# Kernel tuning notes

Hardware: AMD Instinct MI355X
Metric: run time of the kernel (lower is better)

## Reference

```python
import jax, jax.numpy as jnp
import numpy as np

NUM_SEGMENTS = 100000  # number of cycle slots (max cycle id + 1)


def setup_inputs() -> dict:
    key = jax.random.key(0)
    k1, k2, k3 = jax.random.split(key, 3)
    x = jax.random.randint(k1, (100000,), 0, 22, dtype=jnp.int64)
    atom_to_cycle = jax.random.randint(k2, (2, 600000), 0, NUM_SEGMENTS, dtype=jnp.int64)
    emb_weight = jax.random.normal(k3, (22, 128), dtype=jnp.float32)  # Embedding(22, hidden_dim)
    return {"x": x, "atom_to_cycle": atom_to_cycle, "emb_weight": emb_weight}


def reference(x, atom_to_cycle, emb_weight):
    # x: [N] int atom codes; atom_to_cycle: [2, E]; emb_weight: [22, D]
    h = emb_weight[x]                       # [N, D] embedding lookup
    gathered = h[atom_to_cycle[0]]          # [E, D] gather by atom index
    # scatter_sum over cycle ids -> [NUM_SEGMENTS, D]
    out = jax.ops.segment_sum(gathered, atom_to_cycle[1], num_segments=NUM_SEGMENTS)
    return out
```

## Files before the change

### kernel.cpp

```cpp
#include <hip/hip_runtime.h>
#include <stdint.h>

#define KCODES 22
#define KW     11

__global__ void zero_hist(uint32_t* __restrict__ cnt, int nwords4) {
    int i = blockIdx.x * blockDim.x + threadIdx.x;
    if (i < nwords4) {
        ((uint4*)cnt)[i] = make_uint4(0u, 0u, 0u, 0u);
    }
}

__global__ void count_edges(const int* __restrict__ a2c,
                            const int* __restrict__ x,
                            uint32_t* __restrict__ cnt, int E) {
    int e = blockIdx.x * blockDim.x + threadIdx.x;
    if (e < E) {
        int atom = a2c[e];
        int cyc  = a2c[E + e];
        int code = x[atom];
        atomicAdd(&cnt[cyc * KW + (code >> 1)], 1u << ((code & 1) * 16));
    }
}

__global__ __launch_bounds__(256) void expand_out(
        const uint32_t* __restrict__ cnt,
        const float* __restrict__ emb,
        float* __restrict__ out, int num_seg) {
    __shared__ float4 semb[KCODES][32];
    for (int i = threadIdx.x; i < KCODES * 32; i += blockDim.x) {
        semb[i >> 5][i & 31] = ((const float4*)emb)[i];
    }
    __syncthreads();

    const int d4  = threadIdx.x & 31;
    const int sub = threadIdx.x >> 5;

    int c = blockIdx.x * 8 + sub;
    if (c < num_seg) {
        const uint32_t* crow = cnt + (size_t)c * KW;
        float4 acc = make_float4(0.f, 0.f, 0.f, 0.f);
#pragma unroll
        for (int w = 0; w < KW; ++w) {
            uint32_t word = crow[w];
            float c0 = (float)(word & 0xFFFFu);
            float c1 = (float)(word >> 16);
            float4 e0 = semb[2 * w][d4];
            float4 e1 = semb[2 * w + 1][d4];
            acc.x += c0 * e0.x + c1 * e1.x;
            acc.y += c0 * e0.y + c1 * e1.y;
            acc.z += c0 * e0.z + c1 * e1.z;
            acc.w += c0 * e0.w + c1 * e1.w;
        }
        ((float4*)out)[(size_t)c * 32 + d4] = acc;
    }
}

__global__ void zero_out_f4(float4* __restrict__ out, int n4) {
    int i = blockIdx.x * blockDim.x + threadIdx.x;
    if (i < n4) out[i] = make_float4(0.f, 0.f, 0.f, 0.f);
}

__global__ void scatter_edges(const int* __restrict__ a2c,
                              const int* __restrict__ x,
                              const float* __restrict__ emb,
                              float* __restrict__ out, int E) {
    int t = blockIdx.x * blockDim.x + threadIdx.x;
    int e = t >> 5;
    int d = (t & 31) * 4;
    if (e < E) {
        int atom = a2c[e];
        int cyc  = a2c[E + e];
        int code = x[atom];
        const float4 ev = ((const float4*)emb)[code * 32 + (d >> 2)];
        float* o = out + (size_t)cyc * 128 + d;
        atomicAdd(o + 0, ev.x);
        atomicAdd(o + 1, ev.y);
        atomicAdd(o + 2, ev.z);
        atomicAdd(o + 3, ev.w);
    }
}

extern "C" void kernel_launch(void* const* d_in, const int* in_sizes, int n_in,
                              void* d_out, int out_size, void* d_ws, size_t ws_size,
                              hipStream_t stream) {
    const int*   x    = (const int*)d_in[0];
    const int*   a2c  = (const int*)d_in[1];
    const float* emb  = (const float*)d_in[2];
    float*       out  = (float*)d_out;

    const int E       = in_sizes[1] / 2;
    const int D       = in_sizes[2] / KCODES;
    const int num_seg = out_size / D;

    const size_t need = (size_t)num_seg * KW * sizeof(uint32_t);

    if (ws_size >= need) {
        uint32_t* cnt = (uint32_t*)d_ws;
        const int nwords  = num_seg * KW;
        const int nwords4 = (nwords + 3) / 4;

        zero_hist<<<(nwords4 + 255) / 256, 256, 0, stream>>>(cnt, nwords4);
        count_edges<<<(E + 255) / 256, 256, 0, stream>>>(a2c, x, cnt, E);
        expand_out<<<(num_seg + 7) / 8, 256, 0, stream>>>(cnt, emb, out, num_seg);
    } else {
        int n4 = out_size / 4;
        zero_out_f4<<<(n4 + 255) / 256, 256, 0, stream>>>((float4*)out, n4);
        long long threads = (long long)E * 32;
        int blocks = (int)((threads + 255) / 256);
        scatter_edges<<<blocks, 256, 0, stream>>>(a2c, x, emb, out, E);
    }
    (void)n_in; (void)D;
}
```

Before: 116.3 us.

## Pad histogram rows, vectorize edge counting, register-cache embeddings in expand

Pads each cycle's packed count row to 12 words so the expand kernel can read it with three 16-byte loads. The edge-counting kernel now handles four edges per thread using int4 loads, and the custom zero kernel is replaced by hipMemsetAsync. The expand kernel keeps all 22 embedding float4s in registers instead of shared memory, drops the barrier, and runs as a grid-stride loop capped at 2048 blocks. The extra padding word raises workspace traffic, and the 88 registers per thread used for the embedding table may lower occupancy.

```diff
diff --git a/kernel.cpp b/kernel.cpp
--- a/kernel.cpp
+++ b/kernel.cpp
@@ -2,24 +2,36 @@
 #include <stdint.h>
 
 #define KCODES 22
-#define KW     11
+#define KW     12
 
-__global__ void zero_hist(uint32_t* __restrict__ cnt, int nwords4) {
+__global__ void count_edges4(const int* __restrict__ a2c,
+                             const int* __restrict__ x,
+                             uint32_t* __restrict__ cnt, int E) {
     int i = blockIdx.x * blockDim.x + threadIdx.x;
-    if (i < nwords4) {
-        ((uint4*)cnt)[i] = make_uint4(0u, 0u, 0u, 0u);
+    int E4 = E >> 2;
+    if (i < E4) {
+        int4 a = ((const int4*)a2c)[i];
+        int4 c = ((const int4*)(a2c + E))[i];
+        uint32_t k0 = (uint32_t)x[a.x];
+        uint32_t k1 = (uint32_t)x[a.y];
+        uint32_t k2 = (uint32_t)x[a.z];
+        uint32_t k3 = (uint32_t)x[a.w];
+        atomicAdd(&cnt[(size_t)c.x * KW + (k0 >> 1)], 1u << ((k0 & 1) << 4));
+        atomicAdd(&cnt[(size_t)c.y * KW + (k1 >> 1)], 1u << ((k1 & 1) << 4));
+        atomicAdd(&cnt[(size_t)c.z * KW + (k2 >> 1)], 1u << ((k2 & 1) << 4));
+        atomicAdd(&cnt[(size_t)c.w * KW + (k3 >> 1)], 1u << ((k3 & 1) << 4));
     }
 }
 
-__global__ void count_edges(const int* __restrict__ a2c,
-                            const int* __restrict__ x,
-                            uint32_t* __restrict__ cnt, int E) {
+__global__ void count_edges1(const int* __restrict__ a2c,
+                             const int* __restrict__ x,
+                             uint32_t* __restrict__ cnt, int E) {
     int e = blockIdx.x * blockDim.x + threadIdx.x;
     if (e < E) {
         int atom = a2c[e];
         int cyc  = a2c[E + e];
-        int code = x[atom];
-        atomicAdd(&cnt[cyc * KW + (code >> 1)], 1u << ((code & 1) * 16));
+        uint32_t code = (uint32_t)x[atom];
+        atomicAdd(&cnt[(size_t)cyc * KW + (code >> 1)], 1u << ((code & 1) << 4));
     }
 }
 
@@ -27,30 +39,30 @@
         const uint32_t* __restrict__ cnt,
         const float* __restrict__ emb,
         float* __restrict__ out, int num_seg) {
-    __shared__ float4 semb[KCODES][32];
-    for (int i = threadIdx.x; i < KCODES * 32; i += blockDim.x) {
-        semb[i >> 5][i & 31] = ((const float4*)emb)[i];
-    }
-    __syncthreads();
-
     const int d4  = threadIdx.x & 31;
     const int sub = threadIdx.x >> 5;
 
-    int c = blockIdx.x * 8 + sub;
-    if (c < num_seg) {
-        const uint32_t* crow = cnt + (size_t)c * KW;
+    float4 e[KCODES];
+#pragma unroll
+    for (int k = 0; k < KCODES; ++k)
+        e[k] = ((const float4*)emb)[k * 32 + d4];
+
+    for (int c = blockIdx.x * 8 + sub; c < num_seg; c += gridDim.x * 8) {
+        const uint4* crow = (const uint4*)(cnt + (size_t)c * KW);
+        uint4 w0 = crow[0], w1 = crow[1], w2 = crow[2];
+        uint32_t wv[12] = {w0.x, w0.y, w0.z, w0.w,
+                           w1.x, w1.y, w1.z, w1.w,
+                           w2.x, w2.y, w2.z, w2.w};
         float4 acc = make_float4(0.f, 0.f, 0.f, 0.f);
 #pragma unroll
-        for (int w = 0; w < KW; ++w) {
-            uint32_t word = crow[w];
-            float c0 = (float)(word & 0xFFFFu);
-            float c1 = (float)(word >> 16);
-            float4 e0 = semb[2 * w][d4];
-            float4 e1 = semb[2 * w + 1][d4];
-            acc.x += c0 * e0.x + c1 * e1.x;
-            acc.y += c0 * e0.y + c1 * e1.y;
-            acc.z += c0 * e0.z + c1 * e1.z;
-            acc.w += c0 * e0.w + c1 * e1.w;
+        for (int w = 0; w < 11; ++w) {
+            float c0 = (float)(wv[w] & 0xFFFFu);
+            float c1 = (float)(wv[w] >> 16);
+            float4 e0 = e[2 * w], e1 = e[2 * w + 1];
+            acc.x = fmaf(c1, e1.x, fmaf(c0, e0.x, acc.x));
+            acc.y = fmaf(c1, e1.y, fmaf(c0, e0.y, acc.y));
+            acc.z = fmaf(c1, e1.z, fmaf(c0, e0.z, acc.z));
+            acc.w = fmaf(c1, e1.w, fmaf(c0, e0.w, acc.w));
         }
         ((float4*)out)[(size_t)c * 32 + d4] = acc;
     }
@@ -97,12 +109,19 @@
 
     if (ws_size >= need) {
         uint32_t* cnt = (uint32_t*)d_ws;
-        const int nwords  = num_seg * KW;
-        const int nwords4 = (nwords + 3) / 4;
 
-        zero_hist<<<(nwords4 + 255) / 256, 256, 0, stream>>>(cnt, nwords4);
-        count_edges<<<(E + 255) / 256, 256, 0, stream>>>(a2c, x, cnt, E);
-        expand_out<<<(num_seg + 7) / 8, 256, 0, stream>>>(cnt, emb, out, num_seg);
+        hipMemsetAsync(cnt, 0, need, stream);
+
+        if ((E & 3) == 0) {
+            int E4 = E >> 2;
+            count_edges4<<<(E4 + 255) / 256, 256, 0, stream>>>(a2c, x, cnt, E);
+        } else {
+            count_edges1<<<(E + 255) / 256, 256, 0, stream>>>(a2c, x, cnt, E);
+        }
+
+        int blocks = (num_seg + 7) / 8;
+        if (blocks > 2048) blocks = 2048;
+        expand_out<<<blocks, 256, 0, stream>>>(cnt, emb, out, num_seg);
     } else {
         int n4 = out_size / 4;
         zero_out_f4<<<(n4 + 255) / 256, 256, 0, stream>>>((float4*)out, n4);
```

After: 114.5 us. Within noise of the previous version (-1.6%).
